# Performance work log

Measured on AMD Instinct MI355X. Metric: run time of the kernel, lower is better.

The kernel has to match this reference:

```python
import jax, jax.numpy as jnp
import numpy as np

N = 50000      # nodes
E = 800000     # edges (avg degree 16)
IN_DIM, HID, OUT = 128, 128, 64
EPS = 1e-5     # BatchNorm1d eps


def setup_inputs() -> dict:
    key = jax.random.key(0)
    ks = jax.random.split(key, 8)
    x = jax.random.normal(ks[0], (N, IN_DIM), jnp.float32)
    edge_index = jax.random.randint(ks[1], (2, E), 0, N, dtype=jnp.int32)
    def lin(k, i, o):
        return jax.random.normal(k, (i, o), jnp.float32) / np.sqrt(i).astype(np.float32)
    return {
        "x": x,
        "edge_index": edge_index,
        "W1": lin(ks[2], IN_DIM, HID), "b1": jnp.zeros((HID,), jnp.float32),
        "g1": jnp.ones((HID,), jnp.float32), "beta1": jnp.zeros((HID,), jnp.float32),
        "W2": lin(ks[3], HID, HID), "b2": jnp.zeros((HID,), jnp.float32),
        "g2": jnp.ones((HID,), jnp.float32), "beta2": jnp.zeros((HID,), jnp.float32),
        "W3": lin(ks[4], HID, OUT), "b3": jnp.zeros((OUT,), jnp.float32),
    }


def reference(x, edge_index, W1, b1, g1, beta1, W2, b2, g2, beta2, W3, b3):
    # GCNConv normalization: add self-loops, sym norm D^-1/2 (A+I) D^-1/2
    loops = jnp.arange(N, dtype=edge_index.dtype)
    src = jnp.concatenate([edge_index[0], loops])  # message sources
    dst = jnp.concatenate([edge_index[1], loops])  # aggregation targets
    deg = jax.ops.segment_sum(jnp.ones_like(dst, jnp.float32), dst, num_segments=N)
    dis = jnp.where(deg > 0, jax.lax.rsqrt(jnp.maximum(deg, 1.0)), 0.0)
    norm = dis[src] * dis[dst]  # [E+N]

    def conv(h, W, b):
        h = h @ W  # lin before propagation (PyG GCNConv)
        agg = jax.ops.segment_sum(h[src] * norm[:, None], dst, num_segments=N)
        return agg + b  # bias after aggregation

    def bn(h, g, beta):
        # training-mode BatchNorm1d: batch stats over node dim (biased var)
        m = h.mean(axis=0)
        v = h.var(axis=0)
        return g * (h - m) * jax.lax.rsqrt(v + EPS) + beta

    h = jax.nn.relu(bn(conv(x, W1, b1), g1, beta1))   # dropout deterministic (identity)
    h = jax.nn.relu(bn(conv(h, W2, b2), g2, beta2))
    h = conv(h, W3, b3)
    return jax.nn.log_softmax(h, axis=-1)
```

## Files before the change

kernel.cpp:

```cpp
#include <hip/hip_runtime.h>
#include <hip/hip_fp16.h>
#include <math.h>

#define N_NODES 50000
#define N_EDGES 800000
#define BN_EPS 1e-5f
#define CAP 64
#define NPART 256
#define PART 196
#define CHUNK_CAP 48

typedef _Float16 f16x8 __attribute__((ext_vector_type(8)));
typedef _Float16 f16x4 __attribute__((ext_vector_type(4)));
typedef float f32x4 __attribute__((ext_vector_type(4)));

constexpr int GB = (N_NODES + 63) / 64;
constexpr int AB = (N_NODES + 3) / 4;
constexpr int EPB = N_EDGES / NPART;

__global__ __launch_bounds__(256) void setup_partA_k(
    const int* __restrict__ ei, unsigned int* __restrict__ chunk, int* __restrict__ cntT,
    const float* __restrict__ W1, const float* __restrict__ W2, const float* __restrict__ W3,
    __half* __restrict__ Wt1, __half* __restrict__ Wt2, __half* __restrict__ Wt3,
    float* __restrict__ sums) {
    if (blockIdx.x < NPART) {
        __shared__ int cnt[NPART];
        int tid = threadIdx.x, b = blockIdx.x;
        cnt[tid] = 0;
        __syncthreads();
        int lo = b * EPB, hi = lo + EPB;
        for (int e = lo + tid; e < hi; e += 256) {
            int src = ei[e], dst = ei[N_EDGES + e];
            int p = dst / PART;
            int pos = atomicAdd(&cnt[p], 1);
            if (pos < CHUNK_CAP)
                chunk[(unsigned)((b << 8) + p) * CHUNK_CAP + pos] =
                    ((unsigned)dst << 16) | (unsigned)src;
        }
        __syncthreads();
        cntT[tid * NPART + b] = min(cnt[tid], CHUNK_CAP);
    } else {
        int i = (blockIdx.x - NPART) * 256 + threadIdx.x;
        if (i < 512) sums[i] = 0.f;
        if (i < 16384) {
            int k = i >> 7, m = i & 127;
            Wt1[m * 128 + k] = __float2half(W1[i]);
            Wt2[m * 128 + k] = __float2half(W2[i]);
        }
        if (i < 8192) {
            int k = i >> 6, m = i & 63;
            Wt3[m * 128 + k] = __float2half(W3[i]);
        }
    }
}

template <int M, int AF32, int FUSE, int DSCALE>
__device__ __forceinline__ void gemm_body(int bid, int tid,
                                          const void* __restrict__ Av,
                                          const __half* __restrict__ Wt,
                                          const float* __restrict__ sums,
                                          const float* __restrict__ g,
                                          const float* __restrict__ beta,
                                          const int* __restrict__ fil,
                                          __half* __restrict__ out) {
    constexpr int NF = M / 32;
    int wid = tid >> 6, lane = tid & 63;

    int rbase = bid * 64 + (wid >> 1) * 32;
    int ncol0 = (wid & 1) * (M / 2);
    int koff = (lane >> 4) * 8;

    int arow[2];
#pragma unroll
    for (int mi = 0; mi < 2; ++mi) {
        int r = rbase + mi * 16 + (lane & 15);
        arow[mi] = (r < N_NODES) ? r : (N_NODES - 1);
    }

    f32x4 acc[2][NF];
#pragma unroll
    for (int mi = 0; mi < 2; ++mi)
#pragma unroll
        for (int ni = 0; ni < NF; ++ni) acc[mi][ni] = (f32x4)(0.f);

#pragma unroll
    for (int k0 = 0; k0 < 128; k0 += 32) {
        float scv[8], shv[8];
        if constexpr (FUSE) {
#pragma unroll
            for (int j = 0; j < 8; ++j) {
                int k = k0 + koff + j;
                float mn = sums[k] * (1.0f / N_NODES);
                float vr = sums[128 + k] * (1.0f / N_NODES) - mn * mn;
                float sc = g[k] * rsqrtf(vr + BN_EPS);
                scv[j] = sc;
                shv[j] = beta[k] - mn * sc;
            }
        }
        f16x8 a[2], b[NF];
#pragma unroll
        for (int mi = 0; mi < 2; ++mi) {
            if constexpr (AF32) {
                const float* Af = (const float*)Av + (size_t)arow[mi] * 128 + k0 + koff;
                float4 p0 = *(const float4*)Af;
                float4 p1 = *(const float4*)(Af + 4);
                a[mi][0] = (_Float16)p0.x; a[mi][1] = (_Float16)p0.y;
                a[mi][2] = (_Float16)p0.z; a[mi][3] = (_Float16)p0.w;
                a[mi][4] = (_Float16)p1.x; a[mi][5] = (_Float16)p1.y;
                a[mi][6] = (_Float16)p1.z; a[mi][7] = (_Float16)p1.w;
            } else {
                f16x8 raw = *(const f16x8*)((const __half*)Av + (size_t)arow[mi] * 128 + k0 + koff);
                if constexpr (FUSE) {
#pragma unroll
                    for (int j = 0; j < 8; ++j)
                        a[mi][j] = (_Float16)fmaxf((float)raw[j] * scv[j] + shv[j], 0.f);
                } else {
                    a[mi] = raw;
                }
            }
        }
#pragma unroll
        for (int ni = 0; ni < NF; ++ni)
            b[ni] = *(const f16x8*)(Wt + (size_t)(ncol0 + ni * 16 + (lane & 15)) * 128 + k0 + koff);
#pragma unroll
        for (int mi = 0; mi < 2; ++mi)
#pragma unroll
            for (int ni = 0; ni < NF; ++ni)
                acc[mi][ni] = __builtin_amdgcn_mfma_f32_16x16x32_f16(b[ni], a[mi], acc[mi][ni], 0, 0, 0);
    }

    int cg = lane >> 4;
#pragma unroll
    for (int mi = 0; mi < 2; ++mi) {
        int grow = rbase + mi * 16 + (lane & 15);
        if (grow < N_NODES) {
            float ds = DSCALE ? rsqrtf((float)fil[grow] + 1.f) : 1.0f;
#pragma unroll
            for (int ni = 0; ni < NF; ++ni) {
                f16x4 hv;
#pragma unroll
                for (int q = 0; q < 4; ++q) hv[q] = (_Float16)(acc[mi][ni][q] * ds);
                *(f16x4*)(out + (size_t)grow * M + ncol0 + ni * 16 + cg * 4) = hv;
            }
        }
    }
}

template <int M, int AF32, int FUSE, int DSCALE>
__global__ __launch_bounds__(256) void mfma_gemm_k(const void* __restrict__ Av,
                                                   const __half* __restrict__ Wt,
                                                   const float* __restrict__ sums,
                                                   const float* __restrict__ g,
                                                   const float* __restrict__ beta,
                                                   const int* __restrict__ fil,
                                                   __half* __restrict__ out) {
    gemm_body<M, AF32, FUSE, DSCALE>(blockIdx.x, threadIdx.x, Av, Wt, sums, g, beta, fil, out);
}

__global__ __launch_bounds__(256) void partB_gemm1_k(const float* __restrict__ x,
                                                     const __half* __restrict__ Wt1,
                                                     __half* __restrict__ outh,
                                                     const unsigned int* __restrict__ chunk,
                                                     const int* __restrict__ cntT,
                                                     int* __restrict__ fil,
                                                     unsigned short* __restrict__ bkt) {
    if (blockIdx.x < NPART) {
        __shared__ int cur[PART];
        int p = blockIdx.x, tid = threadIdx.x;
        int dst0 = p * PART;
        for (int i = tid; i < PART; i += 256) cur[i] = 0;
        __syncthreads();
        int n = cntT[p * NPART + tid];
        const unsigned int* cp = chunk + (unsigned)((tid << 8) + p) * CHUNK_CAP;
        int i = 0;
        for (; i + 4 <= n; i += 4) {
            uint4 u4 = *(const uint4*)(cp + i);
#pragma unroll
            for (int j = 0; j < 4; ++j) {
                unsigned u = (j == 0) ? u4.x : (j == 1) ? u4.y : (j == 2) ? u4.z : u4.w;
                int dst = u >> 16, src = u & 0xffff;
                int pos = atomicAdd(&cur[dst - dst0], 1);
                if (pos < CAP) bkt[(size_t)dst * CAP + pos] = (unsigned short)src;
            }
        }
        for (; i < n; ++i) {
            unsigned u = cp[i];
            int dst = u >> 16, src = u & 0xffff;
            int pos = atomicAdd(&cur[dst - dst0], 1);
            if (pos < CAP) bkt[(size_t)dst * CAP + pos] = (unsigned short)src;
        }
        __syncthreads();
        for (int i2 = tid; i2 < PART; i2 += 256) {
            int d = dst0 + i2;
            if (d < N_NODES) fil[d] = cur[i2];
        }
    } else {
        gemm_body<128, 1, 0, 0>(blockIdx.x - NPART, threadIdx.x, x, Wt1, nullptr, nullptr,
                                nullptr, nullptr, outh);
    }
}

template <int SRCDIS>
__global__ __launch_bounds__(256) void aggh_k(const __half* __restrict__ hs,
                                              const int* __restrict__ fil,
                                              const unsigned short* __restrict__ bkt,
                                              const float* __restrict__ bias,
                                              __half* __restrict__ out) {
    int dst = blockIdx.x * 4 + (threadIdx.x >> 6);
    if (dst >= N_NODES) return;
    int lane = threadIdx.x & 63;
    int qw = lane >> 4, li = lane & 15;
    int cnt = fil[dst];
    int n = min(cnt, CAP);
    float dd = rsqrtf((float)cnt + 1.f);
    const f16x8* h8 = (const f16x8*)hs;

    float acc[8];
    {
        f16x8 sv = h8[(size_t)dst * 16 + li];
        float selfw = (qw == 0) ? (SRCDIS ? dd : 1.f) : 0.f;
#pragma unroll
        for (int j = 0; j < 8; ++j) acc[j] = selfw * (float)sv[j];
    }

    const unsigned short* bp = bkt + (size_t)dst * CAP;
    int e = 0;
    for (; e + 8 <= n; e += 8) {
        ushort4 ua = *(const ushort4*)(bp + e);
        ushort4 ub = *(const ushort4*)(bp + e + 4);
        int sa = (qw == 0) ? ua.x : (qw == 1) ? ua.y : (qw == 2) ? ua.z : ua.w;
        int sb = (qw == 0) ? ub.x : (qw == 1) ? ub.y : (qw == 2) ? ub.z : ub.w;
        f16x8 va = h8[(size_t)sa * 16 + li];
        f16x8 vb = h8[(size_t)sb * 16 + li];
        float wa = 1.f, wb = 1.f;
        if constexpr (SRCDIS) {
            wa = rsqrtf((float)fil[sa] + 1.f);
            wb = rsqrtf((float)fil[sb] + 1.f);
        }
#pragma unroll
        for (int j = 0; j < 8; ++j) acc[j] += wa * (float)va[j] + wb * (float)vb[j];
    }
    for (; e + 4 <= n; e += 4) {
        ushort4 u = *(const ushort4*)(bp + e);
        int s = (qw == 0) ? u.x : (qw == 1) ? u.y : (qw == 2) ? u.z : u.w;
        f16x8 v = h8[(size_t)s * 16 + li];
        float w = 1.f;
        if constexpr (SRCDIS) w = rsqrtf((float)fil[s] + 1.f);
#pragma unroll
        for (int j = 0; j < 8; ++j) acc[j] += w * (float)v[j];
    }
    if (e < n) {
        int rem = n - e;
        ushort4 u = *(const ushort4*)(bp + e);
        int s = (qw == 0) ? u.x : (qw == 1) ? u.y : (qw == 2) ? u.z : u.w;
        if (qw < rem) {
            f16x8 v = h8[(size_t)s * 16 + li];
            float w = 1.f;
            if constexpr (SRCDIS) w = rsqrtf((float)fil[s] + 1.f);
#pragma unroll
            for (int j = 0; j < 8; ++j) acc[j] += w * (float)v[j];
        }
    }

#pragma unroll
    for (int j = 0; j < 8; ++j) {
        acc[j] += __shfl_xor(acc[j], 16);
        acc[j] += __shfl_xor(acc[j], 32);
    }

    if (qw == 0) {
        float bv[8];
        *(float4*)bv = *(const float4*)(bias + li * 8);
        *(float4*)(bv + 4) = *(const float4*)(bias + li * 8 + 4);
        f16x8 o;
#pragma unroll
        for (int j = 0; j < 8; ++j) o[j] = (_Float16)(dd * acc[j] + bv[j]);
        *(f16x8*)(out + (size_t)dst * 128 + li * 8) = o;
    }
}

__global__ __launch_bounds__(256) void stats_k(const __half* __restrict__ h,
                                               float* __restrict__ sum, float* __restrict__ sq) {
    __shared__ float ssum[128], ssq[128];
    int tid = threadIdx.x;
    if (tid < 128) { ssum[tid] = 0.f; ssq[tid] = 0.f; }
    __syncthreads();
    float s[8], q[8];
#pragma unroll
    for (int j = 0; j < 8; ++j) { s[j] = 0.f; q[j] = 0.f; }
    const int total = N_NODES * 16;
    int stride = gridDim.x * blockDim.x;
    for (int i = blockIdx.x * blockDim.x + tid; i < total; i += stride) {
        f16x8 v = ((const f16x8*)h)[i];
#pragma unroll
        for (int j = 0; j < 8; ++j) {
            float f = (float)v[j];
            s[j] += f;
            q[j] += f * f;
        }
    }
#pragma unroll
    for (int j = 0; j < 8; ++j) {
        s[j] += __shfl_xor(s[j], 16); s[j] += __shfl_xor(s[j], 32);
        q[j] += __shfl_xor(q[j], 16); q[j] += __shfl_xor(q[j], 32);
    }
    int lane = tid & 63;
    if (lane < 16) {
        int c0 = lane * 8;
#pragma unroll
        for (int j = 0; j < 8; ++j) {
            atomicAdd(&ssum[c0 + j], s[j]);
            atomicAdd(&ssq[c0 + j], q[j]);
        }
    }
    __syncthreads();
    if (tid < 128) {
        atomicAdd(&sum[tid], ssum[tid]);
        atomicAdd(&sq[tid], ssq[tid]);
    }
}

__global__ __launch_bounds__(256) void agg64sm_k(const __half* __restrict__ hs,
                                                 const int* __restrict__ fil,
                                                 const unsigned short* __restrict__ bkt,
                                                 const float* __restrict__ bias,
                                                 float* __restrict__ out) {
    int dst = blockIdx.x * 4 + (threadIdx.x >> 6);
    if (dst >= N_NODES) return;
    int lane = threadIdx.x & 63;
    int qw = lane >> 4, li = lane & 15;
    int cnt = fil[dst];
    int n = min(cnt, CAP);
    float dd = rsqrtf((float)cnt + 1.f);
    const f16x4* h4 = (const f16x4*)hs;

    float acc[4];
    {
        f16x4 sv = h4[(size_t)dst * 16 + li];
        float selfw = (qw == 0) ? 1.f : 0.f;
#pragma unroll
        for (int j = 0; j < 4; ++j) acc[j] = selfw * (float)sv[j];
    }

    const unsigned short* bp = bkt + (size_t)dst * CAP;
    int e = 0;
    for (; e + 8 <= n; e += 8) {
        ushort4 ua = *(const ushort4*)(bp + e);
        ushort4 ub = *(const ushort4*)(bp + e + 4);
        int sa = (qw == 0) ? ua.x : (qw == 1) ? ua.y : (qw == 2) ? ua.z : ua.w;
        int sb = (qw == 0) ? ub.x : (qw == 1) ? ub.y : (qw == 2) ? ub.z : ub.w;
        f16x4 va = h4[(size_t)sa * 16 + li];
        f16x4 vb = h4[(size_t)sb * 16 + li];
#pragma unroll
        for (int j = 0; j < 4; ++j) acc[j] += (float)va[j] + (float)vb[j];
    }
    for (; e + 4 <= n; e += 4) {
        ushort4 u = *(const ushort4*)(bp + e);
        int s = (qw == 0) ? u.x : (qw == 1) ? u.y : (qw == 2) ? u.z : u.w;
        f16x4 v = h4[(size_t)s * 16 + li];
#pragma unroll
        for (int j = 0; j < 4; ++j) acc[j] += (float)v[j];
    }
    if (e < n) {
        int rem = n - e;
        ushort4 u = *(const ushort4*)(bp + e);
        int s = (qw == 0) ? u.x : (qw == 1) ? u.y : (qw == 2) ? u.z : u.w;
        if (qw < rem) {
            f16x4 v = h4[(size_t)s * 16 + li];
#pragma unroll
            for (int j = 0; j < 4; ++j) acc[j] += (float)v[j];
        }
    }

#pragma unroll
    for (int j = 0; j < 4; ++j) {
        acc[j] += __shfl_xor(acc[j], 16);
        acc[j] += __shfl_xor(acc[j], 32);
    }

    float bv[4];
    *(float4*)bv = *(const float4*)(bias + li * 4);
    float v[4];
#pragma unroll
    for (int j = 0; j < 4; ++j) v[j] = dd * acc[j] + bv[j];

    float m = fmaxf(fmaxf(v[0], v[1]), fmaxf(v[2], v[3]));
#pragma unroll
    for (int off = 8; off; off >>= 1) m = fmaxf(m, __shfl_xor(m, off));
    float p = expf(v[0] - m) + expf(v[1] - m) + expf(v[2] - m) + expf(v[3] - m);
#pragma unroll
    for (int off = 8; off; off >>= 1) p += __shfl_xor(p, off);
    float lse = m + logf(p);

    if (qw == 0) {
        float4 o = make_float4(v[0] - lse, v[1] - lse, v[2] - lse, v[3] - lse);
        *(float4*)(out + (size_t)dst * 64 + li * 4) = o;
    }
}

extern "C" void kernel_launch(void* const* d_in, const int* in_sizes, int n_in,
                              void* d_out, int out_size, void* d_ws, size_t ws_size,
                              hipStream_t stream) {
    const float* x = (const float*)d_in[0];
    const int* ei = (const int*)d_in[1];
    const float* W1 = (const float*)d_in[2];
    const float* b1 = (const float*)d_in[3];
    const float* g1 = (const float*)d_in[4];
    const float* be1 = (const float*)d_in[5];
    const float* W2 = (const float*)d_in[6];
    const float* b2 = (const float*)d_in[7];
    const float* g2 = (const float*)d_in[8];
    const float* be2 = (const float*)d_in[9];
    const float* W3 = (const float*)d_in[10];
    const float* b3 = (const float*)d_in[11];
    float* out = (float*)d_out;

    char* p = (char*)d_ws;
    auto alloc = [&](size_t bytes) {
        void* r = (void*)p;
        p += (bytes + 255) & ~(size_t)255;
        return r;
    };
    int* fil = (int*)alloc(N_NODES * 4);
    unsigned short* bkt = (unsigned short*)alloc((size_t)N_NODES * CAP * 2);
    unsigned int* chunk = (unsigned int*)alloc((size_t)NPART * NPART * CHUNK_CAP * 4);
    int* cntT = (int*)alloc(NPART * NPART * 4);
    float* sums = (float*)alloc(512 * 4);
    __half* Wt1 = (__half*)alloc(128 * 128 * 2);
    __half* Wt2 = (__half*)alloc(128 * 128 * 2);
    __half* Wt3 = (__half*)alloc(64 * 128 * 2);
    __half* bufP = (__half*)alloc((size_t)N_NODES * 128 * 2);
    __half* bufQ = (__half*)alloc((size_t)N_NODES * 128 * 2);

    setup_partA_k<<<NPART + 196, 256, 0, stream>>>(ei, chunk, cntT, W1, W2, W3, Wt1, Wt2,
                                                   Wt3, sums);

    partB_gemm1_k<<<NPART + GB, 256, 0, stream>>>(x, Wt1, bufQ, chunk, cntT, fil, bkt);
    aggh_k<1><<<AB, 256, 0, stream>>>(bufQ, fil, bkt, b1, bufP);
    stats_k<<<1024, 256, 0, stream>>>(bufP, sums, sums + 128);

    mfma_gemm_k<128, 0, 1, 1><<<GB, 256, 0, stream>>>(bufP, Wt2, sums, g1, be1, fil, bufQ);
    aggh_k<0><<<AB, 256, 0, stream>>>(bufQ, fil, bkt, b2, bufP);
    stats_k<<<1024, 256, 0, stream>>>(bufP, sums + 256, sums + 384);

    mfma_gemm_k<64, 0, 1, 1><<<GB, 256, 0, stream>>>(bufP, Wt3, sums + 256, g2, be2, fil, bufQ);
    agg64sm_k<<<AB, 256, 0, stream>>>(bufQ, fil, bkt, b3, out);
}
```

Before: 240.9 us.

## Remap aggregation kernels to spread edges across more lanes per wavefront

The 128-wide aggregation kernels now split each node's features into four 32-column slices. Each slice runs in its own block, so the grid grows to 50000 blocks. Within a wavefront, 16 lane groups each gather a different neighbour, processing 16 edges per iteration with predicated tails. The 64-wide output kernel now uses 8 groups of 8 lanes with 8-half vector loads and a log-softmax reduced over 8 lanes. The aim is more memory-level parallelism per node and fewer serial loop iterations, at the cost of redundant index and degree loads across slices, more shuffle reductions, and many more tiny blocks.

```diff
diff --git a/kernel.cpp b/kernel.cpp
--- a/kernel.cpp
+++ b/kernel.cpp
@@ -15,7 +15,6 @@
 typedef float f32x4 __attribute__((ext_vector_type(4)));
 
 constexpr int GB = (N_NODES + 63) / 64;
-constexpr int AB = (N_NODES + 3) / 4;
 constexpr int EPB = N_EDGES / NPART;
 
 __global__ __launch_bounds__(256) void setup_partA_k(
@@ -206,76 +205,58 @@
                                               const unsigned short* __restrict__ bkt,
                                               const float* __restrict__ bias,
                                               __half* __restrict__ out) {
-    int dst = blockIdx.x * 4 + (threadIdx.x >> 6);
-    if (dst >= N_NODES) return;
+    int bid = blockIdx.x;
+    int sub = bid & 7;
+    int slice = sub >> 1;
+    int hf = sub & 1;
+    int dst = (bid >> 3) * 8 + hf * 4 + (threadIdx.x >> 6);
     int lane = threadIdx.x & 63;
-    int qw = lane >> 4, li = lane & 15;
+    int g = lane >> 2, l = lane & 3;
     int cnt = fil[dst];
     int n = min(cnt, CAP);
     float dd = rsqrtf((float)cnt + 1.f);
     const f16x8* h8 = (const f16x8*)hs;
+    int col = slice * 4 + l;
 
     float acc[8];
     {
-        f16x8 sv = h8[(size_t)dst * 16 + li];
-        float selfw = (qw == 0) ? (SRCDIS ? dd : 1.f) : 0.f;
+        f16x8 sv = h8[(size_t)dst * 16 + col];
+        float selfw = (g == 0) ? (SRCDIS ? dd : 1.f) : 0.f;
 #pragma unroll
         for (int j = 0; j < 8; ++j) acc[j] = selfw * (float)sv[j];
     }
 
     const unsigned short* bp = bkt + (size_t)dst * CAP;
-    int e = 0;
-    for (; e + 8 <= n; e += 8) {
-        ushort4 ua = *(const ushort4*)(bp + e);
-        ushort4 ub = *(const ushort4*)(bp + e + 4);
-        int sa = (qw == 0) ? ua.x : (qw == 1) ? ua.y : (qw == 2) ? ua.z : ua.w;
-        int sb = (qw == 0) ? ub.x : (qw == 1) ? ub.y : (qw == 2) ? ub.z : ub.w;
-        f16x8 va = h8[(size_t)sa * 16 + li];
-        f16x8 vb = h8[(size_t)sb * 16 + li];
-        float wa = 1.f, wb = 1.f;
-        if constexpr (SRCDIS) {
-            wa = rsqrtf((float)fil[sa] + 1.f);
-            wb = rsqrtf((float)fil[sb] + 1.f);
-        }
-#pragma unroll
-        for (int j = 0; j < 8; ++j) acc[j] += wa * (float)va[j] + wb * (float)vb[j];
-    }
-    for (; e + 4 <= n; e += 4) {
-        ushort4 u = *(const ushort4*)(bp + e);
-        int s = (qw == 0) ? u.x : (qw == 1) ? u.y : (qw == 2) ? u.z : u.w;
-        f16x8 v = h8[(size_t)s * 16 + li];
-        float w = 1.f;
-        if constexpr (SRCDIS) w = rsqrtf((float)fil[s] + 1.f);
+    for (int e0 = 0; e0 < n; e0 += 16) {
+        int idx = e0 + g;
+        bool act = idx < n;
+        int s = act ? bp[idx] : dst;
+        f16x8 v = h8[(size_t)s * 16 + col];
+        float w;
+        if constexpr (SRCDIS)
+            w = act ? rsqrtf((float)fil[s] + 1.f) : 0.f;
+        else
+            w = act ? 1.f : 0.f;
 #pragma unroll
         for (int j = 0; j < 8; ++j) acc[j] += w * (float)v[j];
     }
-    if (e < n) {
-        int rem = n - e;
-        ushort4 u = *(const ushort4*)(bp + e);
-        int s = (qw == 0) ? u.x : (qw == 1) ? u.y : (qw == 2) ? u.z : u.w;
-        if (qw < rem) {
-            f16x8 v = h8[(size_t)s * 16 + li];
-            float w = 1.f;
-            if constexpr (SRCDIS) w = rsqrtf((float)fil[s] + 1.f);
-#pragma unroll
-            for (int j = 0; j < 8; ++j) acc[j] += w * (float)v[j];
-        }
-    }
 
 #pragma unroll
     for (int j = 0; j < 8; ++j) {
+        acc[j] += __shfl_xor(acc[j], 4);
+        acc[j] += __shfl_xor(acc[j], 8);
         acc[j] += __shfl_xor(acc[j], 16);
         acc[j] += __shfl_xor(acc[j], 32);
     }
 
-    if (qw == 0) {
+    if (g == 0) {
         float bv[8];
-        *(float4*)bv = *(const float4*)(bias + li * 8);
-        *(float4*)(bv + 4) = *(const float4*)(bias + li * 8 + 4);
+        *(float4*)bv = *(const float4*)(bias + slice * 32 + l * 8);
+        *(float4*)(bv + 4) = *(const float4*)(bias + slice * 32 + l * 8 + 4);
         f16x8 o;
 #pragma unroll
         for (int j = 0; j < 8; ++j) o[j] = (_Float16)(dd * acc[j] + bv[j]);
-        *(f16x8*)(out + (size_t)dst * 128 + li * 8) = o;
+        *(f16x8*)(out + (size_t)dst * 128 + slice * 32 + l * 8) = o;
     }
 }
 
@@ -328,73 +309,64 @@
     int dst = blockIdx.x * 4 + (threadIdx.x >> 6);
     if (dst >= N_NODES) return;
     int lane = threadIdx.x & 63;
-    int qw = lane >> 4, li = lane & 15;
+    int g = lane >> 3, l = lane & 7;
     int cnt = fil[dst];
     int n = min(cnt, CAP);
     float dd = rsqrtf((float)cnt + 1.f);
-    const f16x4* h4 = (const f16x4*)hs;
-
-    float acc[4];
+    const f16x8* h8 = (const f16x8*)hs;
+
+    float acc[8];
     {
-        f16x4 sv = h4[(size_t)dst * 16 + li];
-        float selfw = (qw == 0) ? 1.f : 0.f;
-#pragma unroll
-        for (int j = 0; j < 4; ++j) acc[j] = selfw * (float)sv[j];
+        f16x8 sv = h8[(size_t)dst * 8 + l];
+        float selfw = (g == 0) ? 1.f : 0.f;
+#pragma unroll
+        for (int j = 0; j < 8; ++j) acc[j] = selfw * (float)sv[j];
     }
 
     const unsigned short* bp = bkt + (size_t)dst * CAP;
-    int e = 0;
-    for (; e + 8 <= n; e += 8) {
-        ushort4 ua = *(const ushort4*)(bp + e);
-        ushort4 ub = *(const ushort4*)(bp + e + 4);
-        int sa = (qw == 0) ? ua.x : (qw == 1) ? ua.y : (qw == 2) ? ua.z : ua.w;
-        int sb = (qw == 0) ? ub.x : (qw == 1) ? ub.y : (qw == 2) ? ub.z : ub.w;
-        f16x4 va = h4[(size_t)sa * 16 + li];
-        f16x4 vb = h4[(size_t)sb * 16 + li];
-#pragma unroll
-        for (int j = 0; j < 4; ++j) acc[j] += (float)va[j] + (float)vb[j];
-    }
-    for (; e + 4 <= n; e += 4) {
-        ushort4 u = *(const ushort4*)(bp + e);
-        int s = (qw == 0) ? u.x : (qw == 1) ? u.y : (qw == 2) ? u.z : u.w;
-        f16x4 v = h4[(size_t)s * 16 + li];
-#pragma unroll
-        for (int j = 0; j < 4; ++j) acc[j] += (float)v[j];
-    }
-    if (e < n) {
-        int rem = n - e;
-        ushort4 u = *(const ushort4*)(bp + e);
-        int s = (qw == 0) ? u.x : (qw == 1) ? u.y : (qw == 2) ? u.z : u.w;
-        if (qw < rem) {
-            f16x4 v = h4[(size_t)s * 16 + li];
-#pragma unroll
-            for (int j = 0; j < 4; ++j) acc[j] += (float)v[j];
-        }
-    }
-
-#pragma unroll
-    for (int j = 0; j < 4; ++j) {
+    for (int e0 = 0; e0 < n; e0 += 8) {
+        int idx = e0 + g;
+        bool act = idx < n;
+        int s = act ? bp[idx] : dst;
+        f16x8 v = h8[(size_t)s * 8 + l];
+        float w = act ? 1.f : 0.f;
+#pragma unroll
+        for (int j = 0; j < 8; ++j) acc[j] += w * (float)v[j];
+    }
+
+#pragma unroll
+    for (int j = 0; j < 8; ++j) {
+        acc[j] += __shfl_xor(acc[j], 8);
         acc[j] += __shfl_xor(acc[j], 16);
         acc[j] += __shfl_xor(acc[j], 32);
     }
 
-    float bv[4];
-    *(float4*)bv = *(const float4*)(bias + li * 4);
-    float v[4];
-#pragma unroll
-    for (int j = 0; j < 4; ++j) v[j] = dd * acc[j] + bv[j];
-
-    float m = fmaxf(fmaxf(v[0], v[1]), fmaxf(v[2], v[3]));
-#pragma unroll
-    for (int off = 8; off; off >>= 1) m = fmaxf(m, __shfl_xor(m, off));
-    float p = expf(v[0] - m) + expf(v[1] - m) + expf(v[2] - m) + expf(v[3] - m);
-#pragma unroll
-    for (int off = 8; off; off >>= 1) p += __shfl_xor(p, off);
+    float bv[8];
+    *(float4*)bv = *(const float4*)(bias + l * 8);
+    *(float4*)(bv + 4) = *(const float4*)(bias + l * 8 + 4);
+    float v[8];
+#pragma unroll
+    for (int j = 0; j < 8; ++j) v[j] = dd * acc[j] + bv[j];
+
+    float m = v[0];
+#pragma unroll
+    for (int j = 1; j < 8; ++j) m = fmaxf(m, v[j]);
+    m = fmaxf(m, __shfl_xor(m, 1));
+    m = fmaxf(m, __shfl_xor(m, 2));
+    m = fmaxf(m, __shfl_xor(m, 4));
+    float p = 0.f;
+#pragma unroll
+    for (int j = 0; j < 8; ++j) p += expf(v[j] - m);
+    p += __shfl_xor(p, 1);
+    p += __shfl_xor(p, 2);
+    p += __shfl_xor(p, 4);
     float lse = m + logf(p);
 
-    if (qw == 0) {
-        float4 o = make_float4(v[0] - lse, v[1] - lse, v[2] - lse, v[3] - lse);
-        *(float4*)(out + (size_t)dst * 64 + li * 4) = o;
+    if (g == 0) {
+        float4 o0 = make_float4(v[0] - lse, v[1] - lse, v[2] - lse, v[3] - lse);
+        float4 o1 = make_float4(v[4] - lse, v[5] - lse, v[6] - lse, v[7] - lse);
+        *(float4*)(out + (size_t)dst * 64 + l * 8) = o0;
+        *(float4*)(out + (size_t)dst * 64 + l * 8 + 4) = o1;
     }
 }
 
@@ -436,13 +408,13 @@
                                                    Wt3, sums);
 
     partB_gemm1_k<<<NPART + GB, 256, 0, stream>>>(x, Wt1, bufQ, chunk, cntT, fil, bkt);
-    aggh_k<1><<<AB, 256, 0, stream>>>(bufQ, fil, bkt, b1, bufP);
+    aggh_k<1><<<50000, 256, 0, stream>>>(bufQ, fil, bkt, b1, bufP);
     stats_k<<<1024, 256, 0, stream>>>(bufP, sums, sums + 128);
 
     mfma_gemm_k<128, 0, 1, 1><<<GB, 256, 0, stream>>>(bufP, Wt2, sums, g1, be1, fil, bufQ);
-    aggh_k<0><<<AB, 256, 0, stream>>>(bufQ, fil, bkt, b2, bufP);
+    aggh_k<0><<<50000, 256, 0, stream>>>(bufQ, fil, bkt, b2, bufP);
     stats_k<<<1024, 256, 0, stream>>>(bufP, sums + 256, sums + 384);
 
     mfma_gemm_k<64, 0, 1, 1><<<GB, 256, 0, stream>>>(bufP, Wt3, sums + 256, g2, be2, fil, bufQ);
-    agg64sm_k<<<AB, 256, 0, stream>>>(bufQ, fil, bkt, b3, out);
-}
+    agg64sm_k<<<(N_NODES + 3) / 4, 256, 0, stream>>>(bufQ, fil, bkt, b3, out);
+}
```

New measurement: 312.6 us. 29.8% more time.
